# Kernel tuning notes

Hardware: AMD Instinct MI355X
Metric: run time of the kernel (lower is better)

## Reference

```python
import jax, jax.numpy as jnp
import numpy as np

NEG_SLOPE = 0.2
BN_EPS = 1e-5


def _gat(x, src, dst, W, a_src, a_dst, b, concat):
    """PyG GATConv (eval mode, self-loops already in src/dst)."""
    N = x.shape[0]
    H, C = a_src.shape
    h = (x @ W).reshape(N, H, C)                      # [N,H,C]
    s = (h * a_src).sum(-1)                           # [N,H] per-node src score
    d = (h * a_dst).sum(-1)                           # [N,H] per-node dst score
    e = jax.nn.leaky_relu(s[src] + d[dst], NEG_SLOPE)  # [E,H]
    m = jax.ops.segment_max(e, dst, num_segments=N)   # segment softmax over dst
    ex = jnp.exp(e - m[dst])
    denom = jax.ops.segment_sum(ex, dst, num_segments=N)
    alpha = ex / denom[dst]                           # [E,H]
    out = jax.ops.segment_sum(alpha[:, :, None] * h[src], dst, num_segments=N)  # [N,H,C]
    out = out.reshape(N, H * C) if concat else out.mean(axis=1)
    return out + b


def _bn(x, g, beta, rm, rv):
    return (x - rm) * (g / jnp.sqrt(rv + BN_EPS)) + beta


def setup_inputs() -> dict:
    key = jax.random.key(0)
    ks = jax.random.split(key, 32)
    N, E, IN, HID, H, NC = 50000, 400000, 768, 128, 4, 2
    d = {}
    d['x'] = jax.random.normal(ks[0], (N, IN), jnp.float32)
    d['edge_index'] = jax.random.randint(ks[1], (2, E), 0, N, jnp.int64)

    def lin(k, fan_in, shape):
        return jax.random.normal(k, shape, jnp.float32) * (1.0 / np.sqrt(fan_in))

    # layer 1: in=768 -> 4 heads x 128, concat
    d['W1'] = lin(ks[2], IN, (IN, H * HID)); d['a1s'] = lin(ks[3], HID, (H, HID))
    d['a1d'] = lin(ks[4], HID, (H, HID)); d['b1'] = jnp.zeros((H * HID,), jnp.float32)
    d['g1'] = jax.random.uniform(ks[5], (H * HID,), jnp.float32, 0.5, 1.5)
    d['be1'] = jax.random.normal(ks[6], (H * HID,), jnp.float32) * 0.1
    d['rm1'] = jax.random.normal(ks[7], (H * HID,), jnp.float32) * 0.1
    d['rv1'] = jax.random.uniform(ks[8], (H * HID,), jnp.float32, 0.5, 1.5)
    d['W2'] = lin(ks[9], H * HID, (H * HID, H * HID)); d['a2s'] = lin(ks[10], HID, (H, HID))
    d['a2d'] = lin(ks[11], HID, (H, HID)); d['b2'] = jnp.zeros((H * HID,), jnp.float32)
    d['g2'] = jax.random.uniform(ks[12], (H * HID,), jnp.float32, 0.5, 1.5)
    d['be2'] = jax.random.normal(ks[13], (H * HID,), jnp.float32) * 0.1
    d['rm2'] = jax.random.normal(ks[14], (H * HID,), jnp.float32) * 0.1
    d['rv2'] = jax.random.uniform(ks[15], (H * HID,), jnp.float32, 0.5, 1.5)
    # layer 3: 512 -> 1 head x 128, mean (concat=False)
    d['W3'] = lin(ks[16], H * HID, (H * HID, HID)); d['a3s'] = lin(ks[17], HID, (1, HID))
    d['a3d'] = lin(ks[18], HID, (1, HID)); d['b3'] = jnp.zeros((HID,), jnp.float32)
    d['g3'] = jax.random.uniform(ks[19], (HID,), jnp.float32, 0.5, 1.5)
    d['be3'] = jax.random.normal(ks[20], (HID,), jnp.float32) * 0.1
    d['rm3'] = jax.random.normal(ks[21], (HID,), jnp.float32) * 0.1
    d['rv3'] = jax.random.uniform(ks[22], (HID,), jnp.float32, 0.5, 1.5)
    # classifier 128 -> 2
    d['Wc'] = lin(ks[23], HID, (HID, NC)); d['bc'] = jnp.zeros((NC,), jnp.float32)
    return d


def reference(x, edge_index, W1, a1s, a1d, b1, g1, be1, rm1, rv1,
              W2, a2s, a2d, b2, g2, be2, rm2, rv2,
              W3, a3s, a3d, b3, g3, be3, rm3, rv3, Wc, bc):
    N = x.shape[0]
    loops = jnp.arange(N, dtype=edge_index.dtype)  # GATConv add_self_loops=True
    src = jnp.concatenate([edge_index[0], loops])
    dst = jnp.concatenate([edge_index[1], loops])

    h = _gat(x, src, dst, W1, a1s, a1d, b1, concat=True)
    h = jax.nn.elu(_bn(h, g1, be1, rm1, rv1))          # dropout: eval mode (identity)
    h = _gat(h, src, dst, W2, a2s, a2d, b2, concat=True)
    h = jax.nn.elu(_bn(h, g2, be2, rm2, rv2))
    h = _gat(h, src, dst, W3, a3s, a3d, b3, concat=False)
    h = jax.nn.elu(_bn(h, g3, be3, rm3, rv3))
    return h @ Wc + bc                                  # [N, 2] logits
```

## Files before the change

kernel.cpp:

```cpp
#include <hip/hip_runtime.h>
#include <hip/hip_bf16.h>
#include <math.h>

constexpr int IN_F = 768;
constexpr float NEG_SLOPE = 0.2f;
constexpr float BN_EPS = 1e-5f;

typedef __attribute__((ext_vector_type(8))) short short8;
typedef __attribute__((ext_vector_type(4))) float f32x4;

__device__ inline float bf2f(unsigned short u) {
    unsigned int x = ((unsigned int)u) << 16;
    return __uint_as_float(x);
}
__device__ inline unsigned short f2bf(float f) {
    __hip_bfloat16 h = __float2bfloat16(f);
    return *(unsigned short*)&h;
}
__device__ inline void gload_lds16(const unsigned short* g, unsigned short* l) {
    __builtin_amdgcn_global_load_lds(
        (const __attribute__((address_space(1))) void*)g,
        (__attribute__((address_space(3))) void*)l, 16, 0, 0);
}


__global__ void init_counts(int* __restrict__ count, int* __restrict__ cursor, int N) {
    int i = blockIdx.x * blockDim.x + threadIdx.x;
    if (i < N) { count[i] = 1; cursor[i] = 0; }
}

__global__ void count_edges(const int* __restrict__ dst, int E, int* __restrict__ count) {
    int e = blockIdx.x * blockDim.x + threadIdx.x;
    if (e < E) atomicAdd(&count[dst[e]], 1);
}

__global__ void scan_counts(const int* __restrict__ count, int* __restrict__ row_start, int N) {
    __shared__ int wsum[17];
    __shared__ int carry;
    int tid = threadIdx.x;
    int lane = tid & 63, w = tid >> 6;
    if (tid == 0) carry = 0;
    __syncthreads();
    for (int base = 0; base < N; base += 4096) {
        int idx = base + tid * 4;
        int v0 = (idx + 0 < N) ? count[idx + 0] : 0;
        int v1 = (idx + 1 < N) ? count[idx + 1] : 0;
        int v2 = (idx + 2 < N) ? count[idx + 2] : 0;
        int v3 = (idx + 3 < N) ? count[idx + 3] : 0;
        int tsum = v0 + v1 + v2 + v3;
        int x = tsum;
        #pragma unroll
        for (int off = 1; off < 64; off <<= 1) {
            int y = __shfl_up(x, off, 64);
            if (lane >= off) x += y;
        }
        if (lane == 63) wsum[w] = x;
        __syncthreads();
        if (tid == 0) {
            int r = 0;
            for (int i = 0; i < 16; i++) { int t = wsum[i]; wsum[i] = r; r += t; }
            wsum[16] = r;
        }
        __syncthreads();
        int excl = carry + wsum[w] + (x - tsum);
        if (idx + 0 < N) row_start[idx + 0] = excl;
        if (idx + 1 < N) row_start[idx + 1] = excl + v0;
        if (idx + 2 < N) row_start[idx + 2] = excl + v0 + v1;
        if (idx + 3 < N) row_start[idx + 3] = excl + v0 + v1 + v2;
        __syncthreads();
        if (tid == 0) carry += wsum[16];
        __syncthreads();
    }
    if (tid == 0) row_start[N] = carry;
}

__global__ void scatter_edges(const int* __restrict__ srcA, const int* __restrict__ dstA,
                              int E, int N, const int* __restrict__ row_start,
                              int* __restrict__ cursor, int* __restrict__ col,
                              int* __restrict__ dstn) {
    int i = blockIdx.x * blockDim.x + threadIdx.x;
    if (i < E) {
        int d = dstA[i];
        int pos = row_start[d] + atomicAdd(&cursor[d], 1);
        col[pos] = srcA[i];
        dstn[pos] = d;
    } else if (i < E + N) {
        int n = i - E;
        int pos = row_start[n] + atomicAdd(&cursor[n], 1);
        col[pos] = n;
        dstn[pos] = n;
    }
}


__global__ void cast_all(const float* __restrict__ x, unsigned short* __restrict__ xb, long xq,
                         const float* __restrict__ W1, const float* __restrict__ W2,
                         const float* __restrict__ W3, unsigned short* __restrict__ Wt1,
                         unsigned short* __restrict__ Wt2, unsigned short* __restrict__ Wt3) {
    long t = (long)blockIdx.x * blockDim.x + threadIdx.x;
    const int S1 = 768 * 512, S2 = 512 * 512, S3 = 512 * 128;
    if (t < xq) {
        long i = t * 4;
        float4 v = *(const float4*)&x[i];
        *(ushort2*)&xb[i] = make_ushort2(f2bf(v.x), f2bf(v.y));
        *(ushort2*)&xb[i + 2] = make_ushort2(f2bf(v.z), f2bf(v.w));
    } else {
        long j = t - xq;
        if (j < S1) {
            int k = (int)j / 512, n = (int)j % 512;
            Wt1[(size_t)n * 768 + k] = f2bf(W1[j]);
        } else if (j < S1 + S2) {
            int jj = (int)(j - S1);
            int k = jj / 512, n = jj % 512;
            Wt2[(size_t)n * 512 + k] = f2bf(W2[jj]);
        } else if (j < S1 + S2 + S3) {
            int jj = (int)(j - S1 - S2);
            int k = jj / 128, n = jj % 128;
            Wt3[(size_t)n * 512 + k] = f2bf(W3[jj]);
        }
    }
}


__global__ __launch_bounds__(256, 3) void gemm_bf16(const unsigned short* __restrict__ A,
                                                    const unsigned short* __restrict__ Wt,
                                                    unsigned short* __restrict__ C,
                                                    const float* __restrict__ a_s,
                                                    const float* __restrict__ a_d,
                                                    float* __restrict__ s2,
                                                    float* __restrict__ d2,
                                                    int M, int Nc, int K, int H) {
    __shared__ __align__(16) unsigned short As[128 * 64];
    __shared__ __align__(16) unsigned short Bs[128 * 64];
    const int tid = threadIdx.x;
    const int lane = tid & 63;
    const int wave = tid >> 6;
    const int wm = wave >> 1, wn = wave & 1;

    const int l = blockIdx.x;
    const int x = l & 7;
    const int t0 = l >> 3;
    const int HT = Nc >> 7;
    const int by = (HT == 4) ? (t0 & 3) : 0;
    const int g  = (HT == 4) ? (t0 >> 2) : t0;
    const int rb = g * 8 + x;
    const int row0 = rb * 128, col0 = by * 128;
    if (row0 >= M) return;

    f32x4 acc[4][4];
    #pragma unroll
    for (int i = 0; i < 4; i++)
        #pragma unroll
        for (int j = 0; j < 4; j++)
            acc[i][j] = (f32x4){0.f, 0.f, 0.f, 0.f};

    const int ldm = tid >> 3;
    const int kpart = (((tid & 7) ^ ((tid >> 3) & 7)) * 8);
    const int fr = lane & 15;
    const int quad = lane >> 4;

    for (int k0 = 0; k0 < K; k0 += 64) {
        __syncthreads();
        #pragma unroll
        for (int i = 0; i < 4; i++) {
            int gr = row0 + i * 32 + ldm; if (gr >= M) gr = M - 1;
            gload_lds16(A + (size_t)gr * K + k0 + kpart, &As[i * 2048 + tid * 8]);
            int n = col0 + i * 32 + ldm;
            gload_lds16(Wt + (size_t)n * K + k0 + kpart, &Bs[i * 2048 + tid * 8]);
        }
        __syncthreads();
        #pragma unroll
        for (int s = 0; s < 2; s++) {
            const int slot8 = (((s << 2) + quad) ^ (fr & 7)) * 8;
            short8 a[4], b[4];
            #pragma unroll
            for (int tt = 0; tt < 4; tt++) {
                a[tt] = *(const short8*)&As[(wm * 64 + tt * 16 + fr) * 64 + slot8];
                b[tt] = *(const short8*)&Bs[(wn * 64 + tt * 16 + fr) * 64 + slot8];
            }
            #pragma unroll
            for (int mi = 0; mi < 4; mi++)
                #pragma unroll
                for (int ni = 0; ni < 4; ni++)
                    acc[mi][ni] = __builtin_amdgcn_mfma_f32_16x16x32_bf16(
                        a[mi], b[ni], acc[mi][ni], 0, 0, 0);
        }
    }

    const int rbase = row0 + wm * 64 + quad * 4;
    const int cbase = col0 + wn * 64 + fr;
    #pragma unroll
    for (int mi = 0; mi < 4; mi++) {
        #pragma unroll
        for (int reg = 0; reg < 4; reg++) {
            int r = rbase + mi * 16 + reg;
            if (r < M) {
                #pragma unroll
                for (int ni = 0; ni < 4; ni++)
                    C[(size_t)r * Nc + cbase + ni * 16] = f2bf(acc[mi][ni][reg]);
            }
        }
    }

    float asv[4], adv[4];
    #pragma unroll
    for (int ni = 0; ni < 4; ni++) {
        int c = by * 128 + wn * 64 + ni * 16 + fr;
        asv[ni] = a_s[c];
        adv[ni] = a_d[c];
    }
    float ps[4][4], pd[4][4];
    #pragma unroll
    for (int mi = 0; mi < 4; mi++)
        #pragma unroll
        for (int reg = 0; reg < 4; reg++) {
            float t = 0.f, u = 0.f;
            #pragma unroll
            for (int ni = 0; ni < 4; ni++) {
                t += acc[mi][ni][reg] * asv[ni];
                u += acc[mi][ni][reg] * adv[ni];
            }
            ps[mi][reg] = t;
            pd[mi][reg] = u;
        }
    #pragma unroll
    for (int off = 1; off <= 8; off <<= 1)
        #pragma unroll
        for (int mi = 0; mi < 4; mi++)
            #pragma unroll
            for (int reg = 0; reg < 4; reg++) {
                ps[mi][reg] += __shfl_xor(ps[mi][reg], off, 64);
                pd[mi][reg] += __shfl_xor(pd[mi][reg], off, 64);
            }
    float oS = 0.f, oD = 0.f;
    #pragma unroll
    for (int mi = 0; mi < 4; mi++)
        #pragma unroll
        for (int reg = 0; reg < 4; reg++)
            if (fr == mi * 4 + reg) { oS = ps[mi][reg]; oD = pd[mi][reg]; }
    int rw = rbase + (fr >> 2) * 16 + (fr & 3);
    if (rw < M) {
        s2[(size_t)rw * (2 * H) + wn * H + by] = oS;
        d2[(size_t)rw * (2 * H) + wn * H + by] = oD;
    }
}


template <int H>
__global__ void edge_weights(const int* __restrict__ col, const int* __restrict__ dstn,
                             const float* __restrict__ s2, const float* __restrict__ d2,
                             float* __restrict__ wgt, int P) {
    int p = blockIdx.x * blockDim.x + threadIdx.x;
    if (p >= P) return;
    int sn = col[p], dn = dstn[p];
    if (H == 4) {
        float4 sa = *(const float4*)&s2[sn * 8];
        float4 sb = *(const float4*)&s2[sn * 8 + 4];
        float4 da = *(const float4*)&d2[dn * 8];
        float4 db = *(const float4*)&d2[dn * 8 + 4];
        float4 o;
        float e;
        e = sa.x + sb.x + da.x + db.x; e = e > 0.f ? e : NEG_SLOPE * e; o.x = __expf(e);
        e = sa.y + sb.y + da.y + db.y; e = e > 0.f ? e : NEG_SLOPE * e; o.y = __expf(e);
        e = sa.z + sb.z + da.z + db.z; e = e > 0.f ? e : NEG_SLOPE * e; o.z = __expf(e);
        e = sa.w + sb.w + da.w + db.w; e = e > 0.f ? e : NEG_SLOPE * e; o.w = __expf(e);
        *(float4*)&wgt[p * 4] = o;
    } else {
        float e = s2[sn * 2] + s2[sn * 2 + 1] + d2[dn * 2] + d2[dn * 2 + 1];
        e = e > 0.f ? e : NEG_SLOPE * e;
        wgt[p] = __expf(e);
    }
}


__global__ void gat_agg_h4(const unsigned short* __restrict__ h, const float* __restrict__ wgt,
                           const int* __restrict__ row_start, const int* __restrict__ col,
                           const float* __restrict__ bias,
                           const float* __restrict__ gam, const float* __restrict__ beta,
                           const float* __restrict__ rm, const float* __restrict__ rv,
                           unsigned short* __restrict__ out, int N) {
    int lane = threadIdx.x & 63;
    int wv = threadIdx.x >> 6;
    int n = blockIdx.x * 4 + wv;
    if (n >= N) return;
    int beg = row_start[n], end = row_start[n + 1];
    int hh = lane >> 4;
    int ch0 = lane * 8;

    float acc[8] = {0.f, 0.f, 0.f, 0.f, 0.f, 0.f, 0.f, 0.f};
    float denom = 0.f;

    for (int i = beg; i < end; i += 8) {
        int cnt = end - i; cnt = cnt > 8 ? 8 : cnt;
        uint4 raw[8]; float w[8];
        #pragma unroll
        for (int u = 0; u < 8; u++) {
            if (u < cnt) {
                int e = i + u;
                int sn = col[e];
                w[u] = wgt[e * 4 + hh];
                raw[u] = *(const uint4*)&h[(size_t)sn * 512 + ch0];
            }
        }
        #pragma unroll
        for (int u = 0; u < 8; u++) {
            if (u < cnt) {
                denom += w[u];
                acc[0] += w[u] * bf2f((unsigned short)(raw[u].x & 0xffff));
                acc[1] += w[u] * bf2f((unsigned short)(raw[u].x >> 16));
                acc[2] += w[u] * bf2f((unsigned short)(raw[u].y & 0xffff));
                acc[3] += w[u] * bf2f((unsigned short)(raw[u].y >> 16));
                acc[4] += w[u] * bf2f((unsigned short)(raw[u].z & 0xffff));
                acc[5] += w[u] * bf2f((unsigned short)(raw[u].z >> 16));
                acc[6] += w[u] * bf2f((unsigned short)(raw[u].w & 0xffff));
                acc[7] += w[u] * bf2f((unsigned short)(raw[u].w >> 16));
            }
        }
    }
    float inv = 1.f / denom;
    float v[8];
    #pragma unroll
    for (int c = 0; c < 8; c++) {
        int ch = ch0 + c;
        float t = acc[c] * inv + bias[ch];
        t = (t - rm[ch]) * (gam[ch] * rsqrtf(rv[ch] + BN_EPS)) + beta[ch];
        v[c] = t > 0.f ? t : expf(t) - 1.f;
    }
    uint4 p;
    p.x = (unsigned int)f2bf(v[0]) | ((unsigned int)f2bf(v[1]) << 16);
    p.y = (unsigned int)f2bf(v[2]) | ((unsigned int)f2bf(v[3]) << 16);
    p.z = (unsigned int)f2bf(v[4]) | ((unsigned int)f2bf(v[5]) << 16);
    p.w = (unsigned int)f2bf(v[6]) | ((unsigned int)f2bf(v[7]) << 16);
    *(uint4*)&out[(size_t)n * 512 + ch0] = p;
}


__global__ void gat_agg_h1_cls(const unsigned short* __restrict__ h, const float* __restrict__ wgt,
                               const int* __restrict__ row_start, const int* __restrict__ col,
                               const float* __restrict__ bias,
                               const float* __restrict__ gam, const float* __restrict__ beta,
                               const float* __restrict__ rm, const float* __restrict__ rv,
                               const float* __restrict__ Wc, const float* __restrict__ bc,
                               float* __restrict__ out, int N) {
    int lane = threadIdx.x & 63;
    int wv = threadIdx.x >> 6;
    int n = blockIdx.x * 4 + wv;
    if (n >= N) return;
    int beg = row_start[n], end = row_start[n + 1];
    int q = lane >> 4;
    int fl = lane & 15;
    const size_t hoff = fl * 8;

    float acc[8] = {0.f, 0.f, 0.f, 0.f, 0.f, 0.f, 0.f, 0.f};
    float denom = 0.f;

    for (int i = beg; i < end; i += 16) {
        uint4 raw[4]; float w[4];
        #pragma unroll
        for (int u = 0; u < 4; u++) {
            int e0 = i + u * 4 + q;
            w[u] = 0.f;
            raw[u] = make_uint4(0u, 0u, 0u, 0u);
            if (e0 < end) {
                int sn = col[e0];
                w[u] = wgt[e0];
                raw[u] = *(const uint4*)&h[(size_t)sn * 128 + hoff];
            }
        }
        #pragma unroll
        for (int u = 0; u < 4; u++) {
            denom += w[u];
            acc[0] += w[u] * bf2f((unsigned short)(raw[u].x & 0xffff));
            acc[1] += w[u] * bf2f((unsigned short)(raw[u].x >> 16));
            acc[2] += w[u] * bf2f((unsigned short)(raw[u].y & 0xffff));
            acc[3] += w[u] * bf2f((unsigned short)(raw[u].y >> 16));
            acc[4] += w[u] * bf2f((unsigned short)(raw[u].z & 0xffff));
            acc[5] += w[u] * bf2f((unsigned short)(raw[u].z >> 16));
            acc[6] += w[u] * bf2f((unsigned short)(raw[u].w & 0xffff));
            acc[7] += w[u] * bf2f((unsigned short)(raw[u].w >> 16));
        }
    }
    #pragma unroll
    for (int c = 0; c < 8; c++) {
        acc[c] += __shfl_xor(acc[c], 16, 64);
        acc[c] += __shfl_xor(acc[c], 32, 64);
    }
    denom += __shfl_xor(denom, 16, 64);
    denom += __shfl_xor(denom, 32, 64);

    if (q == 0) {
        float inv = 1.f / denom;
        int ch0 = fl * 8;
        float p0 = 0.f, p1 = 0.f;
        #pragma unroll
        for (int c = 0; c < 8; c++) {
            int ch = ch0 + c;
            float t = acc[c] * inv + bias[ch];
            t = (t - rm[ch]) * (gam[ch] * rsqrtf(rv[ch] + BN_EPS)) + beta[ch];
            t = t > 0.f ? t : expf(t) - 1.f;
            p0 += t * Wc[ch * 2 + 0];
            p1 += t * Wc[ch * 2 + 1];
        }
        #pragma unroll
        for (int off = 8; off >= 1; off >>= 1) {
            p0 += __shfl_xor(p0, off, 64);
            p1 += __shfl_xor(p1, off, 64);
        }
        if (fl == 0) {
            out[n * 2 + 0] = p0 + bc[0];
            out[n * 2 + 1] = p1 + bc[1];
        }
    }
}


extern "C" void kernel_launch(void* const* d_in, const int* in_sizes, int n_in,
                              void* d_out, int out_size, void* d_ws, size_t ws_size,
                              hipStream_t stream) {
    const float* x   = (const float*)d_in[0];
    const int*   ei  = (const int*)d_in[1];
    const float* W1  = (const float*)d_in[2];
    const float* a1s = (const float*)d_in[3];
    const float* a1d = (const float*)d_in[4];
    const float* b1  = (const float*)d_in[5];
    const float* gm1 = (const float*)d_in[6];
    const float* be1 = (const float*)d_in[7];
    const float* rm1 = (const float*)d_in[8];
    const float* rv1 = (const float*)d_in[9];
    const float* W2  = (const float*)d_in[10];
    const float* a2s = (const float*)d_in[11];
    const float* a2d = (const float*)d_in[12];
    const float* b2  = (const float*)d_in[13];
    const float* gm2 = (const float*)d_in[14];
    const float* be2 = (const float*)d_in[15];
    const float* rm2 = (const float*)d_in[16];
    const float* rv2 = (const float*)d_in[17];
    const float* W3  = (const float*)d_in[18];
    const float* a3s = (const float*)d_in[19];
    const float* a3d = (const float*)d_in[20];
    const float* b3  = (const float*)d_in[21];
    const float* gm3 = (const float*)d_in[22];
    const float* be3 = (const float*)d_in[23];
    const float* rm3 = (const float*)d_in[24];
    const float* rv3 = (const float*)d_in[25];
    const float* Wc  = (const float*)d_in[26];
    const float* bc  = (const float*)d_in[27];

    int N = in_sizes[0] / IN_F;
    int E = in_sizes[1] / 2;
    int P = E + N;
    const int* srcA = ei;
    const int* dstA = ei + E;

    unsigned short* xb   = (unsigned short*)d_ws;
    unsigned short* hbuf = xb + (size_t)N * 768;
    unsigned short* gbuf = hbuf + (size_t)N * 512;
    float* s2   = (float*)(gbuf + (size_t)N * 512);
    float* d2   = s2 + (size_t)N * 8;
    float* wgt  = d2 + (size_t)N * 8;
    unsigned short* Wt1 = (unsigned short*)(wgt + (size_t)P * 4);
    unsigned short* Wt2 = Wt1 + 512 * 768;
    unsigned short* Wt3 = Wt2 + 512 * 512;
    int* count     = (int*)(Wt3 + 128 * 512);
    int* cursor    = count + N;
    int* row_start = cursor + N;
    int* col       = row_start + N + 1;
    int* dstn      = col + P;

    init_counts<<<(N + 255) / 256, 256, 0, stream>>>(count, cursor, N);
    count_edges<<<(E + 255) / 256, 256, 0, stream>>>(dstA, E, count);
    scan_counts<<<1, 1024, 0, stream>>>(count, row_start, N);
    scatter_edges<<<(E + N + 255) / 256, 256, 0, stream>>>(srcA, dstA, E, N, row_start,
                                                           cursor, col, dstn);
    long xq = (long)N * IN_F / 4;
    long ctot = xq + 768 * 512 + 512 * 512 + 512 * 128;
    cast_all<<<(int)((ctot + 255) / 256), 256, 0, stream>>>(x, xb, xq, W1, W2, W3,
                                                            Wt1, Wt2, Wt3);

    int Mb = (N + 127) / 128;
    int MbP = (Mb + 7) & ~7;
    int Nb4 = (N + 3) / 4;

    gemm_bf16<<<4 * MbP, 256, 0, stream>>>(xb, Wt1, hbuf, a1s, a1d, s2, d2, N, 512, 768, 4);
    edge_weights<4><<<(P + 255) / 256, 256, 0, stream>>>(col, dstn, s2, d2, wgt, P);
    gat_agg_h4<<<Nb4, 256, 0, stream>>>(hbuf, wgt, row_start, col,
                                        b1, gm1, be1, rm1, rv1, gbuf, N);
    gemm_bf16<<<4 * MbP, 256, 0, stream>>>(gbuf, Wt2, hbuf, a2s, a2d, s2, d2, N, 512, 512, 4);
    edge_weights<4><<<(P + 255) / 256, 256, 0, stream>>>(col, dstn, s2, d2, wgt, P);
    gat_agg_h4<<<Nb4, 256, 0, stream>>>(hbuf, wgt, row_start, col,
                                        b2, gm2, be2, rm2, rv2, gbuf, N);
    gemm_bf16<<<MbP, 256, 0, stream>>>(gbuf, Wt3, hbuf, a3s, a3d, s2, d2, N, 128, 512, 1);
    edge_weights<1><<<(P + 255) / 256, 256, 0, stream>>>(col, dstn, s2, d2, wgt, P);
    gat_agg_h1_cls<<<Nb4, 256, 0, stream>>>(hbuf, wgt, row_start, col,
                                            b3, gm3, be3, rm3, rv3, Wc, bc, (float*)d_out, N);
}
```

Before: 660.2 us.

## Fuse edge-weight computation into aggregation kernels and merge init into cast

Removes the three separate edge_weights kernels and computes the leaky-relu/exp attention weight inline in the aggregation kernels from per-node s2/d2 scores. This drops the wgt and dstn buffers and their global writes and reads. The counts/cursor init is folded into cast_all, which now converts 8 floats per thread, and the scan processes 16 elements per thread with vector loads. In exchange, each aggregation kernel does extra exp work and extra gathers of s2 per edge, redundantly across the lanes that handle a head.

New measurement: 662.7 us. No clear change (+0.4%).

```diff
diff --git a/kernel.cpp b/kernel.cpp
--- a/kernel.cpp
+++ b/kernel.cpp
@@ -23,11 +23,6 @@
         (__attribute__((address_space(3))) void*)l, 16, 0, 0);
 }
 
-
-__global__ void init_counts(int* __restrict__ count, int* __restrict__ cursor, int N) {
-    int i = blockIdx.x * blockDim.x + threadIdx.x;
-    if (i < N) { count[i] = 1; cursor[i] = 0; }
-}
 
 __global__ void count_edges(const int* __restrict__ dst, int E, int* __restrict__ count) {
     int e = blockIdx.x * blockDim.x + threadIdx.x;
@@ -41,13 +36,23 @@
     int lane = tid & 63, w = tid >> 6;
     if (tid == 0) carry = 0;
     __syncthreads();
-    for (int base = 0; base < N; base += 4096) {
-        int idx = base + tid * 4;
-        int v0 = (idx + 0 < N) ? count[idx + 0] : 0;
-        int v1 = (idx + 1 < N) ? count[idx + 1] : 0;
-        int v2 = (idx + 2 < N) ? count[idx + 2] : 0;
-        int v3 = (idx + 3 < N) ? count[idx + 3] : 0;
-        int tsum = v0 + v1 + v2 + v3;
+    for (int base = 0; base < N; base += 16384) {
+        int idx = base + tid * 16;
+        int v[16];
+        if (idx + 16 <= N) {
+            #pragma unroll
+            for (int j = 0; j < 4; j++) {
+                int4 t4 = *(const int4*)&count[idx + j * 4];
+                v[j * 4 + 0] = t4.x; v[j * 4 + 1] = t4.y;
+                v[j * 4 + 2] = t4.z; v[j * 4 + 3] = t4.w;
+            }
+        } else {
+            #pragma unroll
+            for (int j = 0; j < 16; j++) v[j] = (idx + j < N) ? count[idx + j] : 0;
+        }
+        int tsum = 0;
+        #pragma unroll
+        for (int j = 0; j < 16; j++) tsum += v[j];
         int x = tsum;
         #pragma unroll
         for (int off = 1; off < 64; off <<= 1) {
@@ -63,10 +68,11 @@
         }
         __syncthreads();
         int excl = carry + wsum[w] + (x - tsum);
-        if (idx + 0 < N) row_start[idx + 0] = excl;
-        if (idx + 1 < N) row_start[idx + 1] = excl + v0;
-        if (idx + 2 < N) row_start[idx + 2] = excl + v0 + v1;
-        if (idx + 3 < N) row_start[idx + 3] = excl + v0 + v1 + v2;
+        #pragma unroll
+        for (int j = 0; j < 16; j++) {
+            if (idx + j < N) row_start[idx + j] = excl;
+            excl += v[j];
+        }
         __syncthreads();
         if (tid == 0) carry += wsum[16];
         __syncthreads();
@@ -76,36 +82,39 @@
 
 __global__ void scatter_edges(const int* __restrict__ srcA, const int* __restrict__ dstA,
                               int E, int N, const int* __restrict__ row_start,
-                              int* __restrict__ cursor, int* __restrict__ col,
-                              int* __restrict__ dstn) {
+                              int* __restrict__ cursor, int* __restrict__ col) {
     int i = blockIdx.x * blockDim.x + threadIdx.x;
     if (i < E) {
         int d = dstA[i];
         int pos = row_start[d] + atomicAdd(&cursor[d], 1);
         col[pos] = srcA[i];
-        dstn[pos] = d;
     } else if (i < E + N) {
         int n = i - E;
         int pos = row_start[n] + atomicAdd(&cursor[n], 1);
         col[pos] = n;
-        dstn[pos] = n;
-    }
-}
-
-
-__global__ void cast_all(const float* __restrict__ x, unsigned short* __restrict__ xb, long xq,
+    }
+}
+
+
+__global__ void cast_all(const float* __restrict__ x, unsigned short* __restrict__ xb, long xq8,
                          const float* __restrict__ W1, const float* __restrict__ W2,
                          const float* __restrict__ W3, unsigned short* __restrict__ Wt1,
-                         unsigned short* __restrict__ Wt2, unsigned short* __restrict__ Wt3) {
+                         unsigned short* __restrict__ Wt2, unsigned short* __restrict__ Wt3,
+                         int* __restrict__ count, int* __restrict__ cursor, int N) {
     long t = (long)blockIdx.x * blockDim.x + threadIdx.x;
     const int S1 = 768 * 512, S2 = 512 * 512, S3 = 512 * 128;
-    if (t < xq) {
-        long i = t * 4;
-        float4 v = *(const float4*)&x[i];
-        *(ushort2*)&xb[i] = make_ushort2(f2bf(v.x), f2bf(v.y));
-        *(ushort2*)&xb[i + 2] = make_ushort2(f2bf(v.z), f2bf(v.w));
+    if (t < xq8) {
+        long i = t * 8;
+        float4 v0 = *(const float4*)&x[i];
+        float4 v1 = *(const float4*)&x[i + 4];
+        uint4 p;
+        p.x = (unsigned int)f2bf(v0.x) | ((unsigned int)f2bf(v0.y) << 16);
+        p.y = (unsigned int)f2bf(v0.z) | ((unsigned int)f2bf(v0.w) << 16);
+        p.z = (unsigned int)f2bf(v1.x) | ((unsigned int)f2bf(v1.y) << 16);
+        p.w = (unsigned int)f2bf(v1.z) | ((unsigned int)f2bf(v1.w) << 16);
+        *(uint4*)&xb[i] = p;
     } else {
-        long j = t - xq;
+        long j = t - xq8;
         if (j < S1) {
             int k = (int)j / 512, n = (int)j % 512;
             Wt1[(size_t)n * 768 + k] = f2bf(W1[j]);
@@ -117,6 +126,9 @@
             int jj = (int)(j - S1 - S2);
             int k = jj / 128, n = jj % 128;
             Wt3[(size_t)n * 512 + k] = f2bf(W3[jj]);
+        } else {
+            long j2 = j - (S1 + S2 + S3);
+            if (j2 < N) { count[j2] = 1; cursor[j2] = 0; }
         }
     }
 }
@@ -246,34 +258,8 @@
 }
 
 
-template <int H>
-__global__ void edge_weights(const int* __restrict__ col, const int* __restrict__ dstn,
-                             const float* __restrict__ s2, const float* __restrict__ d2,
-                             float* __restrict__ wgt, int P) {
-    int p = blockIdx.x * blockDim.x + threadIdx.x;
-    if (p >= P) return;
-    int sn = col[p], dn = dstn[p];
-    if (H == 4) {
-        float4 sa = *(const float4*)&s2[sn * 8];
-        float4 sb = *(const float4*)&s2[sn * 8 + 4];
-        float4 da = *(const float4*)&d2[dn * 8];
-        float4 db = *(const float4*)&d2[dn * 8 + 4];
-        float4 o;
-        float e;
-        e = sa.x + sb.x + da.x + db.x; e = e > 0.f ? e : NEG_SLOPE * e; o.x = __expf(e);
-        e = sa.y + sb.y + da.y + db.y; e = e > 0.f ? e : NEG_SLOPE * e; o.y = __expf(e);
-        e = sa.z + sb.z + da.z + db.z; e = e > 0.f ? e : NEG_SLOPE * e; o.z = __expf(e);
-        e = sa.w + sb.w + da.w + db.w; e = e > 0.f ? e : NEG_SLOPE * e; o.w = __expf(e);
-        *(float4*)&wgt[p * 4] = o;
-    } else {
-        float e = s2[sn * 2] + s2[sn * 2 + 1] + d2[dn * 2] + d2[dn * 2 + 1];
-        e = e > 0.f ? e : NEG_SLOPE * e;
-        wgt[p] = __expf(e);
-    }
-}
-
-
-__global__ void gat_agg_h4(const unsigned short* __restrict__ h, const float* __restrict__ wgt,
+__global__ void gat_agg_h4(const unsigned short* __restrict__ h,
+                           const float* __restrict__ s2, const float* __restrict__ d2,
                            const int* __restrict__ row_start, const int* __restrict__ col,
                            const float* __restrict__ bias,
                            const float* __restrict__ gam, const float* __restrict__ beta,
@@ -286,6 +272,7 @@
     int beg = row_start[n], end = row_start[n + 1];
     int hh = lane >> 4;
     int ch0 = lane * 8;
+    float dh = d2[(size_t)n * 8 + hh] + d2[(size_t)n * 8 + 4 + hh];
 
     float acc[8] = {0.f, 0.f, 0.f, 0.f, 0.f, 0.f, 0.f, 0.f};
     float denom = 0.f;
@@ -298,7 +285,9 @@
             if (u < cnt) {
                 int e = i + u;
                 int sn = col[e];
-                w[u] = wgt[e * 4 + hh];
+                float ev = s2[(size_t)sn * 8 + hh] + s2[(size_t)sn * 8 + 4 + hh] + dh;
+                ev = ev > 0.f ? ev : NEG_SLOPE * ev;
+                w[u] = __expf(ev);
                 raw[u] = *(const uint4*)&h[(size_t)sn * 512 + ch0];
             }
         }
@@ -335,7 +324,8 @@
 }
 
 
-__global__ void gat_agg_h1_cls(const unsigned short* __restrict__ h, const float* __restrict__ wgt,
+__global__ void gat_agg_h1_cls(const unsigned short* __restrict__ h,
+                               const float* __restrict__ s2, const float* __restrict__ d2,
                                const int* __restrict__ row_start, const int* __restrict__ col,
                                const float* __restrict__ bias,
                                const float* __restrict__ gam, const float* __restrict__ beta,
@@ -350,6 +340,7 @@
     int q = lane >> 4;
     int fl = lane & 15;
     const size_t hoff = fl * 8;
+    float dsum = d2[(size_t)n * 2] + d2[(size_t)n * 2 + 1];
 
     float acc[8] = {0.f, 0.f, 0.f, 0.f, 0.f, 0.f, 0.f, 0.f};
     float denom = 0.f;
@@ -363,7 +354,10 @@
             raw[u] = make_uint4(0u, 0u, 0u, 0u);
             if (e0 < end) {
                 int sn = col[e0];
-                w[u] = wgt[e0];
+                float2 sv = *(const float2*)&s2[(size_t)sn * 2];
+                float ev = sv.x + sv.y + dsum;
+                ev = ev > 0.f ? ev : NEG_SLOPE * ev;
+                w[u] = __expf(ev);
                 raw[u] = *(const uint4*)&h[(size_t)sn * 128 + hoff];
             }
         }
@@ -457,40 +451,35 @@
     unsigned short* gbuf = hbuf + (size_t)N * 512;
     float* s2   = (float*)(gbuf + (size_t)N * 512);
     float* d2   = s2 + (size_t)N * 8;
-    float* wgt  = d2 + (size_t)N * 8;
-    unsigned short* Wt1 = (unsigned short*)(wgt + (size_t)P * 4);
+    unsigned short* Wt1 = (unsigned short*)(d2 + (size_t)N * 8);
     unsigned short* Wt2 = Wt1 + 512 * 768;
     unsigned short* Wt3 = Wt2 + 512 * 512;
     int* count     = (int*)(Wt3 + 128 * 512);
     int* cursor    = count + N;
     int* row_start = cursor + N;
     int* col       = row_start + N + 1;
-    int* dstn      = col + P;
-
-    init_counts<<<(N + 255) / 256, 256, 0, stream>>>(count, cursor, N);
+
+    long xq8 = (long)N * IN_F / 8;
+    long ctot = xq8 + 768 * 512 + 512 * 512 + 512 * 128 + N;
+    cast_all<<<(int)((ctot + 255) / 256), 256, 0, stream>>>(x, xb, xq8, W1, W2, W3,
+                                                            Wt1, Wt2, Wt3,
+                                                            count, cursor, N);
     count_edges<<<(E + 255) / 256, 256, 0, stream>>>(dstA, E, count);
     scan_counts<<<1, 1024, 0, stream>>>(count, row_start, N);
     scatter_edges<<<(E + N + 255) / 256, 256, 0, stream>>>(srcA, dstA, E, N, row_start,
-                                                           cursor, col, dstn);
-    long xq = (long)N * IN_F / 4;
-    long ctot = xq + 768 * 512 + 512 * 512 + 512 * 128;
-    cast_all<<<(int)((ctot + 255) / 256), 256, 0, stream>>>(x, xb, xq, W1, W2, W3,
-                                                            Wt1, Wt2, Wt3);
+                                                           cursor, col);
 
     int Mb = (N + 127) / 128;
     int MbP = (Mb + 7) & ~7;
     int Nb4 = (N + 3) / 4;
 
     gemm_bf16<<<4 * MbP, 256, 0, stream>>>(xb, Wt1, hbuf, a1s, a1d, s2, d2, N, 512, 768, 4);
-    edge_weights<4><<<(P + 255) / 256, 256, 0, stream>>>(col, dstn, s2, d2, wgt, P);
-    gat_agg_h4<<<Nb4, 256, 0, stream>>>(hbuf, wgt, row_start, col,
+    gat_agg_h4<<<Nb4, 256, 0, stream>>>(hbuf, s2, d2, row_start, col,
                                         b1, gm1, be1, rm1, rv1, gbuf, N);
     gemm_bf16<<<4 * MbP, 256, 0, stream>>>(gbuf, Wt2, hbuf, a2s, a2d, s2, d2, N, 512, 512, 4);
-    edge_weights<4><<<(P + 255) / 256, 256, 0, stream>>>(col, dstn, s2, d2, wgt, P);
-    gat_agg_h4<<<Nb4, 256, 0, stream>>>(hbuf, wgt, row_start, col,
+    gat_agg_h4<<<Nb4, 256, 0, stream>>>(hbuf, s2, d2, row_start, col,
                                         b2, gm2, be2, rm2, rv2, gbuf, N);
     gemm_bf16<<<MbP, 256, 0, stream>>>(gbuf, Wt3, hbuf, a3s, a3d, s2, d2, N, 128, 512, 1);
-    edge_weights<1><<<(P + 255) / 256, 256, 0, stream>>>(col, dstn, s2, d2, wgt, P);
-    gat_agg_h1_cls<<<Nb4, 256, 0, stream>>>(hbuf, wgt, row_start, col,
+    gat_agg_h1_cls<<<Nb4, 256, 0, stream>>>(hbuf, s2, d2, row_start, col,
                                             b3, gm3, be3, rm3, rv3, Wc, bc, (float*)d_out, N);
 }
```
